# Optimization experiments

Measured on AMD Instinct MI355X. Metric: run time of the kernel, lower is better.

Reference implementation:

```python
import jax, jax.numpy as jnp
import numpy as np

D_MODEL = 512
NUM_HEADS = 8
HEAD_DIM = D_MODEL // NUM_HEADS
ATTN_WINDOW = 256


def setup_inputs() -> dict:
    key = jax.random.key(0)
    ks = jax.random.split(key, 5)
    B, S = 2, 4096
    x = jax.random.normal(ks[0], (B, S, D_MODEL), dtype=jnp.float32)
    s = 1.0 / np.sqrt(D_MODEL)
    qkv_w = jax.random.uniform(ks[1], (3 * D_MODEL, D_MODEL), minval=-s, maxval=s, dtype=jnp.float32)
    qkv_b = jax.random.uniform(ks[2], (3 * D_MODEL,), minval=-s, maxval=s, dtype=jnp.float32)
    out_w = jax.random.uniform(ks[3], (D_MODEL, D_MODEL), minval=-s, maxval=s, dtype=jnp.float32)
    out_b = jax.random.uniform(ks[4], (D_MODEL,), minval=-s, maxval=s, dtype=jnp.float32)
    return {"x": x, "qkv_w": qkv_w, "qkv_b": qkv_b, "out_w": out_w, "out_b": out_b}


def reference(x, qkv_w, qkv_b, out_w, out_b):
    B, S, D = x.shape
    scale = HEAD_DIM ** (-0.5)
    qkv = x @ qkv_w.T + qkv_b                       # [B,S,3D]
    qkv = qkv.reshape(B, S, 3, NUM_HEADS, HEAD_DIM)
    q, k, v = qkv[:, :, 0], qkv[:, :, 1], qkv[:, :, 2]
    scores = jnp.einsum('bthd,bshd->bhts', q, k) * scale  # [B,H,S,S]
    i = jnp.arange(S)[:, None]
    j = jnp.arange(S)[None, :]
    # causal AND within sliding window of size ATTN_WINDOW
    mask = (j <= i) & (j >= i - ATTN_WINDOW)        # [S,S] bool
    scores = jnp.where(mask, scores, -jnp.inf)
    weights = jax.nn.softmax(scores, axis=-1)
    out = jnp.einsum('bhts,bshd->bthd', weights, v).reshape(B, S, D)
    return out @ out_w.T + out_b
```

## Files before the change

kernel.cpp:

```cpp
#include <hip/hip_runtime.h>

#define S_LEN 4096
#define BATCH 2
#define DM 512
#define NH 8
#define DH 64
#define WINDOW 256

typedef __bf16 bf16x8 __attribute__((ext_vector_type(8)));
typedef float f32x4 __attribute__((ext_vector_type(4)));
typedef unsigned short u16x8 __attribute__((ext_vector_type(8)));

typedef const __attribute__((address_space(1))) unsigned int* gas_ptr;
typedef __attribute__((address_space(3))) unsigned int* las_ptr;

#define SCALE_LOG2E 0.1803368801111204f

__device__ __forceinline__ unsigned short f2bf(float f) {
  unsigned int u = __float_as_uint(f);
  u += 0x7fffu + ((u >> 16) & 1u);
  return (unsigned short)(u >> 16);
}

#define N4_X (8192 * 512 / 4)
#define N4_QW (1536 * 512 / 4)
#define N4_OW (512 * 512 / 4)
__global__ __launch_bounds__(256) void convert_all(const float* __restrict__ x,
                                                   const float* __restrict__ qw,
                                                   const float* __restrict__ ow,
                                                   unsigned short* __restrict__ dst) {
  const int i = blockIdx.x * blockDim.x + threadIdx.x;
  const float4* src;
  int off;
  if (i < N4_X) { src = (const float4*)x; off = 0; }
  else if (i < N4_X + N4_QW) { src = (const float4*)qw; off = N4_X; }
  else { src = (const float4*)ow; off = N4_X + N4_QW; }
  const float4 v = src[i - off];
  ushort4 o;
  o.x = f2bf(v.x); o.y = f2bf(v.y); o.z = f2bf(v.z); o.w = f2bf(v.w);
  ((ushort4*)dst)[i] = o;
}

__device__ __forceinline__ void gemm_core(const unsigned short* __restrict__ A,
                                          const unsigned short* __restrict__ Bm,
                                          int m0, int n0,
                                          unsigned short* sA, unsigned short* sB,
                                          f32x4 acc[4][4]) {
  const int t = threadIdx.x;
  const int wave = t >> 6, lane = t & 63;
  const int wr = wave >> 1, wc = wave & 1;
  const int quad = lane >> 4, l16 = lane & 15;

  for (int k0 = 0; k0 < 512; k0 += 32) {
#pragma unroll
    for (int p = 0; p < 2; ++p) {
      const int ci = wave * 128 + p * 64 + lane;
      const int row = ci >> 2, cg = ci & 3;
      const unsigned short* ga = A + (size_t)(m0 + row) * 512 + k0 + cg * 8;
      __builtin_amdgcn_global_load_lds((gas_ptr)(const void*)ga,
                                       (las_ptr)(void*)(sA + wave * 1024 + p * 512), 16, 0, 0);
      const unsigned short* gb = Bm + (size_t)(n0 + row) * 512 + k0 + cg * 8;
      __builtin_amdgcn_global_load_lds((gas_ptr)(const void*)gb,
                                       (las_ptr)(void*)(sB + wave * 1024 + p * 512), 16, 0, 0);
    }
    __syncthreads();
    bf16x8 af[4], bff[4];
#pragma unroll
    for (int i = 0; i < 4; ++i)
      af[i] = *(const bf16x8*)&sA[(wr * 64 + i * 16 + l16) * 32 + quad * 8];
#pragma unroll
    for (int j = 0; j < 4; ++j)
      bff[j] = *(const bf16x8*)&sB[(wc * 64 + j * 16 + l16) * 32 + quad * 8];
#pragma unroll
    for (int i = 0; i < 4; ++i)
#pragma unroll
      for (int j = 0; j < 4; ++j)
        acc[i][j] = __builtin_amdgcn_mfma_f32_16x16x32_bf16(af[i], bff[j], acc[i][j], 0, 0, 0);
    __syncthreads();
  }
}

__global__ __launch_bounds__(256) void gemm_qkv(const unsigned short* __restrict__ xb,
                                                const unsigned short* __restrict__ wb,
                                                const float* __restrict__ bias,
                                                unsigned short* __restrict__ Qb,
                                                unsigned short* __restrict__ Kb,
                                                unsigned short* __restrict__ Vt) {
  __shared__ __align__(16) unsigned short sA[128 * 32];
  __shared__ __align__(16) unsigned short sB[128 * 32];
  f32x4 acc[4][4] = {};
  const int m0 = blockIdx.y * 128, n0 = blockIdx.x * 128;
  gemm_core(xb, wb, m0, n0, sA, sB, acc);

  const int t = threadIdx.x;
  const int wave = t >> 6, lane = t & 63;
  const int wr = wave >> 1, wc = wave & 1;
  const int quad = lane >> 4, l16 = lane & 15;
#pragma unroll
  for (int j = 0; j < 4; ++j) {
    const int n = n0 + wc * 64 + j * 16 + l16;
    const float bv = bias[n];
#pragma unroll
    for (int i = 0; i < 4; ++i) {
      const int mr = m0 + wr * 64 + i * 16 + quad * 4;
      if (n < DM) {
#pragma unroll
        for (int r = 0; r < 4; ++r)
          Qb[(size_t)(mr + r) * DM + n] = f2bf(acc[i][j][r] + bv);
      } else if (n < 2 * DM) {
#pragma unroll
        for (int r = 0; r < 4; ++r)
          Kb[(size_t)(mr + r) * DM + (n - DM)] = f2bf(acc[i][j][r] + bv);
      } else {
        const int d = n & 63, h = (n - 2 * DM) >> 6;
#pragma unroll
        for (int r = 0; r < 4; ++r) {
          const int m = mr + r;
          const int b = m >> 12, s = m & (S_LEN - 1);
          Vt[((size_t)((b * NH + h) * DH + d)) * S_LEN + s] = f2bf(acc[i][j][r] + bv);
        }
      }
    }
  }
}

__global__ __launch_bounds__(256) void gemm_out(const unsigned short* __restrict__ Ab,
                                                const unsigned short* __restrict__ wb,
                                                const float* __restrict__ bias,
                                                float* __restrict__ C) {
  __shared__ __align__(16) unsigned short sA[128 * 32];
  __shared__ __align__(16) unsigned short sB[128 * 32];
  f32x4 acc[4][4] = {};
  const int m0 = blockIdx.y * 128, n0 = blockIdx.x * 128;
  gemm_core(Ab, wb, m0, n0, sA, sB, acc);

  const int t = threadIdx.x;
  const int wave = t >> 6, lane = t & 63;
  const int wr = wave >> 1, wc = wave & 1;
  const int quad = lane >> 4, l16 = lane & 15;
#pragma unroll
  for (int j = 0; j < 4; ++j) {
    const int n = n0 + wc * 64 + j * 16 + l16;
    const float bv = bias[n];
#pragma unroll
    for (int i = 0; i < 4; ++i) {
      const int mr = m0 + wr * 64 + i * 16 + quad * 4;
#pragma unroll
      for (int r = 0; r < 4; ++r)
        C[(size_t)(mr + r) * DM + n] = acc[i][j][r] + bv;
    }
  }
}

__global__ __launch_bounds__(256) void attn_mfma(const unsigned short* __restrict__ Qb,
                                                 const unsigned short* __restrict__ Kb,
                                                 const unsigned short* __restrict__ Vt,
                                                 unsigned short* __restrict__ AO) {
  __shared__ __align__(16) unsigned short Qs[64 * 72];
  __shared__ __align__(16) unsigned short Ks[64 * 72];
  __shared__ __align__(16) unsigned short Vs[64 * 72];
  __shared__ __align__(16) unsigned short Ps[64 * 72];
  const int t = threadIdx.x;
  const int wave = t >> 6, lane = t & 63;
  const int quad = lane >> 4, l16 = lane & 15;
  const int q0 = blockIdx.x * 64, h = blockIdx.y, b = blockIdx.z;

  const unsigned short* Kbase = Kb + (size_t)b * S_LEN * DM + h * DH;
  const unsigned short* Vbase = Vt + (size_t)((b * NH + h) * DH) * S_LEN;

#pragma unroll
  for (int s = 0; s < 2; ++s) {
    const int f = t + 256 * s;
    const int row = f >> 3, cg = f & 7;
    *(u16x8*)&Qs[row * 72 + cg * 8] =
        *(const u16x8*)(Qb + (size_t)(b * S_LEN + q0 + row) * DM + h * DH + cg * 8);
  }

  const int first = (q0 >= WINDOW) ? 0 : (4 - blockIdx.x);

  u16x8 kbuf[2][2], vbuf[2][2];
#define LOAD_CHUNK(c0, p)                                                      \
  do {                                                                         \
    _Pragma("unroll") for (int s = 0; s < 2; ++s) {                            \
      const int f = t + 256 * s;                                               \
      const int row = f >> 3, c8 = f & 7;                                      \
      kbuf[p][s] = *(const u16x8*)(Kbase + (size_t)((c0) + row) * DM + c8 * 8);\
      vbuf[p][s] = *(const u16x8*)(Vbase + (size_t)row * S_LEN + (c0) + c8 * 8);\
    }                                                                          \
  } while (0)

#pragma unroll
  for (int c = 0; c < 5; ++c)
    if (c == first) LOAD_CHUNK(q0 - WINDOW + c * 64, c & 1);

  float m_[4], l_[4];
  f32x4 O[4] = {};
#pragma unroll
  for (int r = 0; r < 4; ++r) { m_[r] = -1e30f; l_[r] = 0.f; }

#pragma unroll
  for (int c = 0; c < 5; ++c) {
    if (c < first) continue;
    const int c0 = q0 - WINDOW + c * 64;
    __syncthreads();
#pragma unroll
    for (int s = 0; s < 2; ++s) {
      const int f = t + 256 * s;
      const int row = f >> 3, c8 = f & 7;
      *(u16x8*)&Ks[row * 72 + c8 * 8] = kbuf[c & 1][s];
      *(u16x8*)&Vs[row * 72 + c8 * 8] = vbuf[c & 1][s];
    }
    if (c < 4) LOAD_CHUNK(c0 + 64, (c + 1) & 1);
    __syncthreads();

    bf16x8 aq0 = *(const bf16x8*)&Qs[(wave * 16 + l16) * 72 + quad * 8];
    bf16x8 aq1 = *(const bf16x8*)&Qs[(wave * 16 + l16) * 72 + 32 + quad * 8];
    f32x4 sc[4];
#pragma unroll
    for (int nt = 0; nt < 4; ++nt) {
      bf16x8 bk0 = *(const bf16x8*)&Ks[(nt * 16 + l16) * 72 + quad * 8];
      bf16x8 bk1 = *(const bf16x8*)&Ks[(nt * 16 + l16) * 72 + 32 + quad * 8];
      f32x4 z = {};
      z = __builtin_amdgcn_mfma_f32_16x16x32_bf16(aq0, bk0, z, 0, 0, 0);
      sc[nt] = __builtin_amdgcn_mfma_f32_16x16x32_bf16(aq1, bk1, z, 0, 0, 0);
    }

    float rmax[4];
#pragma unroll
    for (int r = 0; r < 4; ++r) rmax[r] = -1e30f;
#pragma unroll
    for (int nt = 0; nt < 4; ++nt) {
      const int jj = nt * 16 + l16;
#pragma unroll
      for (int r = 0; r < 4; ++r) {
        const int ii = wave * 16 + quad * 4 + r;
        float v = sc[nt][r] * SCALE_LOG2E;
        if (c == 0) v = (jj >= ii) ? v : -1e30f;
        if (c == 4) v = (jj <= ii) ? v : -1e30f;
        sc[nt][r] = v;
        rmax[r] = fmaxf(rmax[r], v);
      }
    }
#pragma unroll
    for (int off = 1; off <= 8; off <<= 1)
#pragma unroll
      for (int r = 0; r < 4; ++r) rmax[r] = fmaxf(rmax[r], __shfl_xor(rmax[r], off));

    float alpha[4], csum[4];
#pragma unroll
    for (int r = 0; r < 4; ++r) {
      const float mn = fmaxf(m_[r], rmax[r]);
      alpha[r] = exp2f(m_[r] - mn);
      m_[r] = mn;
      float su = 0.f;
#pragma unroll
      for (int nt = 0; nt < 4; ++nt) {
        const float p = exp2f(sc[nt][r] - mn);
        sc[nt][r] = p;
        su += p;
      }
      csum[r] = su;
    }
#pragma unroll
    for (int off = 1; off <= 8; off <<= 1)
#pragma unroll
      for (int r = 0; r < 4; ++r) csum[r] += __shfl_xor(csum[r], off);
#pragma unroll
    for (int r = 0; r < 4; ++r) l_[r] = l_[r] * alpha[r] + csum[r];

#pragma unroll
    for (int nt = 0; nt < 4; ++nt)
#pragma unroll
      for (int r = 0; r < 4; ++r)
        Ps[(wave * 16 + quad * 4 + r) * 72 + nt * 16 + l16] = f2bf(sc[nt][r]);

    bf16x8 ap0 = *(const bf16x8*)&Ps[(wave * 16 + l16) * 72 + quad * 8];
    bf16x8 ap1 = *(const bf16x8*)&Ps[(wave * 16 + l16) * 72 + 32 + quad * 8];
#pragma unroll
    for (int nt = 0; nt < 4; ++nt) {
#pragma unroll
      for (int r = 0; r < 4; ++r) O[nt][r] *= alpha[r];
      bf16x8 bv0 = *(const bf16x8*)&Vs[(nt * 16 + l16) * 72 + quad * 8];
      bf16x8 bv1 = *(const bf16x8*)&Vs[(nt * 16 + l16) * 72 + 32 + quad * 8];
      O[nt] = __builtin_amdgcn_mfma_f32_16x16x32_bf16(ap0, bv0, O[nt], 0, 0, 0);
      O[nt] = __builtin_amdgcn_mfma_f32_16x16x32_bf16(ap1, bv1, O[nt], 0, 0, 0);
    }
  }

#pragma unroll
  for (int r = 0; r < 4; ++r) l_[r] = 1.f / l_[r];
#pragma unroll
  for (int nt = 0; nt < 4; ++nt) {
    const int col = h * DH + nt * 16 + l16;
#pragma unroll
    for (int r = 0; r < 4; ++r) {
      const int m = b * S_LEN + q0 + wave * 16 + quad * 4 + r;
      AO[(size_t)m * DM + col] = f2bf(O[nt][r] * l_[r]);
    }
  }
}

extern "C" void kernel_launch(void* const* d_in, const int* in_sizes, int n_in,
                              void* d_out, int out_size, void* d_ws, size_t ws_size,
                              hipStream_t stream) {
  const float* x = (const float*)d_in[0];
  const float* qkv_w = (const float*)d_in[1];
  const float* qkv_b = (const float*)d_in[2];
  const float* out_w = (const float*)d_in[3];
  const float* out_b = (const float*)d_in[4];
  float* out = (float*)d_out;

  const int M = BATCH * S_LEN;
  unsigned short* ws = (unsigned short*)d_ws;
  unsigned short* xb   = ws;
  unsigned short* wqkv = xb + (size_t)M * DM;
  unsigned short* wout = wqkv + 3 * DM * DM;
  unsigned short* Qb   = wout + DM * DM;
  unsigned short* Kb   = Qb + (size_t)M * DM;
  unsigned short* Vt   = Kb + (size_t)M * DM;
  unsigned short* AO   = Vt + (size_t)M * DM;

  convert_all<<<(N4_X + N4_QW + N4_OW) / 256, 256, 0, stream>>>(x, qkv_w, out_w, xb);

  gemm_qkv<<<dim3(3 * DM / 128, M / 128), 256, 0, stream>>>(xb, wqkv, qkv_b, Qb, Kb, Vt);

  attn_mfma<<<dim3(S_LEN / 64, NH, BATCH), 256, 0, stream>>>(Qb, Kb, Vt, AO);

  gemm_out<<<dim3(DM / 128, M / 128), 256, 0, stream>>>(AO, wout, out_b, out);
}
```

Measured before the change: 149.7 us.

## Widen attention blocks to 128 queries sharing K/V chunks across two wave groups

The attention kernel now processes 128 query rows per block with 512 threads. Two groups of four waves share each staged 64-key K/V chunk, each group covering its own five-chunk window. This cuts redundant K/V global loads and LDS staging per query and halves the number of blocks. In exchange, each block iterates six chunks with one idle group at the ends, uses more LDS, and launches fewer blocks.

```diff
diff --git a/kernel.cpp b/kernel.cpp
--- a/kernel.cpp
+++ b/kernel.cpp
@@ -152,45 +152,44 @@
   }
 }
 
-__global__ __launch_bounds__(256) void attn_mfma(const unsigned short* __restrict__ Qb,
+__global__ __launch_bounds__(512) void attn_mfma(const unsigned short* __restrict__ Qb,
                                                  const unsigned short* __restrict__ Kb,
                                                  const unsigned short* __restrict__ Vt,
                                                  unsigned short* __restrict__ AO) {
-  __shared__ __align__(16) unsigned short Qs[64 * 72];
+  __shared__ __align__(16) unsigned short Qs[128 * 72];
+  __shared__ __align__(16) unsigned short Ps[128 * 72];
   __shared__ __align__(16) unsigned short Ks[64 * 72];
   __shared__ __align__(16) unsigned short Vs[64 * 72];
-  __shared__ __align__(16) unsigned short Ps[64 * 72];
   const int t = threadIdx.x;
   const int wave = t >> 6, lane = t & 63;
   const int quad = lane >> 4, l16 = lane & 15;
-  const int q0 = blockIdx.x * 64, h = blockIdx.y, b = blockIdx.z;
+  const int wgrp = wave >> 2;
+  const int q0 = blockIdx.x * 128, h = blockIdx.y, b = blockIdx.z;
 
   const unsigned short* Kbase = Kb + (size_t)b * S_LEN * DM + h * DH;
   const unsigned short* Vbase = Vt + (size_t)((b * NH + h) * DH) * S_LEN;
 
 #pragma unroll
   for (int s = 0; s < 2; ++s) {
-    const int f = t + 256 * s;
+    const int f = t + 512 * s;
     const int row = f >> 3, cg = f & 7;
     *(u16x8*)&Qs[row * 72 + cg * 8] =
         *(const u16x8*)(Qb + (size_t)(b * S_LEN + q0 + row) * DM + h * DH + cg * 8);
   }
 
-  const int first = (q0 >= WINDOW) ? 0 : (4 - blockIdx.x);
-
-  u16x8 kbuf[2][2], vbuf[2][2];
-#define LOAD_CHUNK(c0, p)                                                      \
-  do {                                                                         \
-    _Pragma("unroll") for (int s = 0; s < 2; ++s) {                            \
-      const int f = t + 256 * s;                                               \
-      const int row = f >> 3, c8 = f & 7;                                      \
-      kbuf[p][s] = *(const u16x8*)(Kbase + (size_t)((c0) + row) * DM + c8 * 8);\
-      vbuf[p][s] = *(const u16x8*)(Vbase + (size_t)row * S_LEN + (c0) + c8 * 8);\
-    }                                                                          \
+  const int bx = blockIdx.x;
+  const int first = (bx >= 2) ? 0 : (4 - 2 * bx);
+
+  const int srow = t >> 3, scg = t & 7;
+  u16x8 kbuf[2], vbuf[2];
+#define LOAD_CHUNK(c0, p)                                                       \
+  do {                                                                          \
+    kbuf[p] = *(const u16x8*)(Kbase + (size_t)((c0) + srow) * DM + scg * 8);    \
+    vbuf[p] = *(const u16x8*)(Vbase + (size_t)srow * S_LEN + (c0) + scg * 8);   \
   } while (0)
 
 #pragma unroll
-  for (int c = 0; c < 5; ++c)
+  for (int c = 0; c < 6; ++c)
     if (c == first) LOAD_CHUNK(q0 - WINDOW + c * 64, c & 1);
 
   float m_[4], l_[4];
@@ -199,19 +198,16 @@
   for (int r = 0; r < 4; ++r) { m_[r] = -1e30f; l_[r] = 0.f; }
 
 #pragma unroll
-  for (int c = 0; c < 5; ++c) {
+  for (int c = 0; c < 6; ++c) {
     if (c < first) continue;
     const int c0 = q0 - WINDOW + c * 64;
     __syncthreads();
-#pragma unroll
-    for (int s = 0; s < 2; ++s) {
-      const int f = t + 256 * s;
-      const int row = f >> 3, c8 = f & 7;
-      *(u16x8*)&Ks[row * 72 + c8 * 8] = kbuf[c & 1][s];
-      *(u16x8*)&Vs[row * 72 + c8 * 8] = vbuf[c & 1][s];
-    }
-    if (c < 4) LOAD_CHUNK(c0 + 64, (c + 1) & 1);
+    *(u16x8*)&Ks[srow * 72 + scg * 8] = kbuf[c & 1];
+    *(u16x8*)&Vs[srow * 72 + scg * 8] = vbuf[c & 1];
+    if (c < 5) LOAD_CHUNK(c0 + 64, (c + 1) & 1);
     __syncthreads();
+
+    if (c < wgrp || c > 4 + wgrp) continue;
 
     bf16x8 aq0 = *(const bf16x8*)&Qs[(wave * 16 + l16) * 72 + quad * 8];
     bf16x8 aq1 = *(const bf16x8*)&Qs[(wave * 16 + l16) * 72 + 32 + quad * 8];
@@ -230,13 +226,13 @@
     for (int r = 0; r < 4; ++r) rmax[r] = -1e30f;
 #pragma unroll
     for (int nt = 0; nt < 4; ++nt) {
-      const int jj = nt * 16 + l16;
+      const int jjl = nt * 16 + l16;
 #pragma unroll
       for (int r = 0; r < 4; ++r) {
-        const int ii = wave * 16 + quad * 4 + r;
+        const int iiRel = (wave & 3) * 16 + quad * 4 + r;
         float v = sc[nt][r] * SCALE_LOG2E;
-        if (c == 0) v = (jj >= ii) ? v : -1e30f;
-        if (c == 4) v = (jj <= ii) ? v : -1e30f;
+        if (c == wgrp) v = (jjl >= iiRel) ? v : -1e30f;
+        if (c == 4 + wgrp) v = (jjl <= iiRel) ? v : -1e30f;
         sc[nt][r] = v;
         rmax[r] = fmaxf(rmax[r], v);
       }
@@ -322,9 +318,9 @@
 
   convert_all<<<(N4_X + N4_QW + N4_OW) / 256, 256, 0, stream>>>(x, qkv_w, out_w, xb);
 
-  gemm_qkv<<<dim3(3 * DM / 128, M / 128), 256, 0, stream>>>(xb, wqkv, qkv_b, Qb, Kb, Vt);
-
-  attn_mfma<<<dim3(S_LEN / 64, NH, BATCH), 256, 0, stream>>>(Qb, Kb, Vt, AO);
-
-  gemm_out<<<dim3(DM / 128, M / 128), 256, 0, stream>>>(AO, wout, out_b, out);
-}
+  gemm_qkv<<<dim3(12, 64), 256, 0, stream>>>(xb, wqkv, qkv_b, Qb, Kb, Vt);
+
+  attn_mfma<<<dim3(S_LEN / 128, NH, BATCH), 512, 0, stream>>>(Qb, Kb, Vt, AO);
+
+  gemm_out<<<dim3(4, 64), 256, 0, stream>>>(AO, wout, out_b, out);
+}
```

Result: no change. 149.1 us (-0.4%).
